# Performance work log

Hardware: AMD Instinct MI355X
Metric: run time of the kernel (lower is better)

The kernel has to match this reference:

```python
import jax, jax.numpy as jnp
import numpy as np

GROUPS = 4
RATIO = 2


def setup_inputs() -> dict:
    key = jax.random.key(0)
    k1, k2, k3 = jax.random.split(key, 3)
    B, C, H, W = 16, 256, 64, 64
    c_out = 2 * GROUPS * RATIO ** 2  # 32
    x = jax.random.normal(k1, (B, C, H, W), dtype=jnp.float32)
    # offset conv: normal_init std=0.001 (full 1x1 conv)
    w_off = jax.random.normal(k2, (c_out, C), dtype=jnp.float32) * 0.001
    b_off = jnp.zeros((c_out,), dtype=jnp.float32)
    # scope conv: grouped 1x1 (groups=4); init is zeros in the module, use tiny
    # random values so sigmoid != exactly 0.5 and the path is exercised
    w_scope = jax.random.normal(k3, (GROUPS, c_out // GROUPS, C // GROUPS), dtype=jnp.float32) * 0.001
    b_scope = jnp.zeros((c_out,), dtype=jnp.float32)
    return {"x": x, "w_off": w_off, "b_off": b_off, "w_scope": w_scope, "b_scope": b_scope}


def _pixel_shuffle(t, r):
    B, C, H, W = t.shape
    Co = C // (r * r)
    t = t.reshape(B, Co, r, r, H, W)
    t = t.transpose(0, 1, 4, 2, 5, 3)  # B, Co, H, r, W, r
    return t.reshape(B, Co, H * r, W * r)


def _bilinear_border(img, ix, iy):
    # img: (c, H, W); ix, iy: (Ho, Wo) pixel coords in input space
    c, H, W = img.shape
    ix = jnp.clip(ix, 0.0, W - 1.0)  # border padding: clamp coordinate
    iy = jnp.clip(iy, 0.0, H - 1.0)
    x0f = jnp.floor(ix)
    y0f = jnp.floor(iy)
    wx = ix - x0f
    wy = iy - y0f
    x0 = jnp.clip(x0f.astype(jnp.int32), 0, W - 1)
    x1 = jnp.clip(x0 + 1, 0, W - 1)
    y0 = jnp.clip(y0f.astype(jnp.int32), 0, H - 1)
    y1 = jnp.clip(y0 + 1, 0, H - 1)
    v00 = img[:, y0, x0]
    v01 = img[:, y0, x1]
    v10 = img[:, y1, x0]
    v11 = img[:, y1, x1]
    return (v00 * (1 - wy) * (1 - wx) + v01 * (1 - wy) * wx
            + v10 * wy * (1 - wx) + v11 * wy * wx)


def reference(x, w_off, b_off, w_scope, b_scope):
    B, C, H, W = x.shape
    g, r = GROUPS, RATIO
    # offset 1x1 conv
    off = jnp.einsum('bihw,oi->bohw', x, w_off) + b_off[None, :, None, None]
    # grouped scope 1x1 conv + sigmoid scaling
    xgc = x.reshape(B, g, C // g, H, W)
    sc = jnp.einsum('bgihw,goi->bgohw', xgc, w_scope).reshape(B, -1, H, W)
    sc = sc + b_scope[None, :, None, None]
    off = jax.nn.sigmoid(sc) * 0.5 * off
    # pixel shuffle to (B, 2*g, Ho, Wo)
    off = _pixel_shuffle(off, r)
    Ho, Wo = H * r, W * r
    # rearrange: x 'b (c grp) h w -> (b grp) c h w'; offset 'b (grp two) h w -> (b grp) h w two'
    cg = C // g
    xg = x.reshape(B, cg, g, H, W).transpose(0, 2, 1, 3, 4).reshape(B * g, cg, H, W)
    og = off.reshape(B, g, 2, Ho, Wo).transpose(0, 1, 3, 4, 2).reshape(B * g, Ho, Wo, 2)
    # sampling grid: centers + offset, normalized by (Wo, Ho), align_corners=False
    posx = jnp.linspace(0.5, Wo - 0.5, Wo, dtype=x.dtype)[None, :]   # (1, Wo)
    posy = jnp.linspace(0.5, Ho - 0.5, Ho, dtype=x.dtype)[:, None]   # (Ho, 1)
    gx = 2.0 * (posx + og[..., 0]) / Wo - 1.0  # (B*g, Ho, Wo)
    gy = 2.0 * (posy + og[..., 1]) / Ho - 1.0
    # unnormalize (align_corners=False): pix = ((g+1)*size - 1) / 2
    ix = ((gx + 1.0) * W - 1.0) * 0.5
    iy = ((gy + 1.0) * H - 1.0) * 0.5
    out = jax.vmap(_bilinear_border)(xg, ix, iy)  # (B*g, cg, Ho, Wo)
    # rearrange back: '(b grp) c h w -> b (c grp) h w'
    out = out.reshape(B, g, cg, Ho, Wo).transpose(0, 2, 1, 3, 4).reshape(B, C, Ho, Wo)
    return out
```

## Files before the change

### kernel.cpp

```cpp
#include <hip/hip_runtime.h>
#include <math.h>

#define B_   16
#define C_   256
#define H_   64
#define W_   64
#define G_   4
#define HO_  128
#define WO_  128
#define HW_  (H_ * W_)
#define HOWO_ (HO_ * WO_)

__constant__ float wconst[8 * 32 * 40];

__global__ __launch_bounds__(256) void prep_kernel(
    const float* __restrict__ w_off,
    const float* __restrict__ w_scope,
    float* __restrict__ wout)
{
    const int k = blockIdx.x * 256 + threadIdx.x;
    if (k >= 8 * 32 * 40) return;
    const int q  = k % 40;
    const int r  = k / 40;
    const int i2 = r & 31;
    const int u  = r >> 5;
    const int v  = u & 3;
    const int hi = u >> 2;
    const int i  = 64 * v + 32 * hi + i2;
    float val;
    if (q < 32) val = w_off[q * 256 + i];
    else        val = w_scope[v * 512 + (q - 32) * 64 + 32 * hi + i2];
    wout[k] = val;
}

__global__ __launch_bounds__(512, 6) void fused_kernel(
    const float* __restrict__ x,
    const float* __restrict__ b_off,
    const float* __restrict__ b_scope,
    float* __restrict__ out)
{
    __shared__ float4 red[8][8][64];
    __shared__ float4 aux[8][64];

    const int tid = threadIdx.x;
    const int u   = __builtin_amdgcn_readfirstlane(tid >> 6);
    const int w   = tid & 63;

    const int bid = ((blockIdx.x & 7) << 7) | (blockIdx.x >> 3);
    const int h   = bid & 63;
    const int b   = bid >> 6;

    const int v   = u & 3;
    const int hi  = u >> 2;

    const float* xq = x + (size_t)b * C_ * HW_ +
                      (size_t)(64 * v + 32 * hi) * HW_ + h * W_ + w;
    const int wbase0 = u * (32 * 40);

    float offp[32];
    float scp[8];
#pragma unroll
    for (int j = 0; j < 32; ++j) offp[j] = 0.f;
#pragma unroll
    for (int j = 0; j < 8; ++j) scp[j] = 0.f;

#pragma unroll 4
    for (int i2 = 0; i2 < 32; ++i2) {
        const float xv = xq[(size_t)i2 * HW_];
        const int wb = wbase0 + i2 * 40;
#pragma unroll
        for (int j = 0; j < 32; ++j) offp[j] += xv * wconst[wb + j];
#pragma unroll
        for (int j = 0; j < 8; ++j)  scp[j] += xv * wconst[wb + 32 + j];
    }

    if (hi) {
#pragma unroll
        for (int j = 0; j < 8; ++j)
            red[4 + v][j][w] = make_float4(offp[4 * j + 0], offp[4 * j + 1],
                                           offp[4 * j + 2], offp[4 * j + 3]);
        aux[2 * v + 0][w] = make_float4(scp[0], scp[1], scp[2], scp[3]);
        aux[2 * v + 1][w] = make_float4(scp[4], scp[5], scp[6], scp[7]);
    }
    __syncthreads();
    if (!hi) {
#pragma unroll
        for (int j = 0; j < 8; ++j) {
            const float4 p = red[4 + v][j][w];
            offp[4 * j + 0] += p.x; offp[4 * j + 1] += p.y;
            offp[4 * j + 2] += p.z; offp[4 * j + 3] += p.w;
        }
        const float4 s0 = aux[2 * v + 0][w];
        const float4 s1 = aux[2 * v + 1][w];
        scp[0] += s0.x; scp[1] += s0.y; scp[2] += s0.z; scp[3] += s0.w;
        scp[4] += s1.x; scp[5] += s1.y; scp[6] += s1.z; scp[7] += s1.w;
#pragma unroll
        for (int j = 0; j < 8; ++j)
            red[v][j][w] = make_float4(offp[4 * j + 0], offp[4 * j + 1],
                                       offp[4 * j + 2], offp[4 * j + 3]);
    }
    __syncthreads();
    if (!hi) {
        float4 a = make_float4(0.f, 0.f, 0.f, 0.f);
        float4 c = make_float4(0.f, 0.f, 0.f, 0.f);
#pragma unroll
        for (int tt = 0; tt < 4; ++tt) {
            const float4 pa = red[tt][2 * v + 0][w];
            const float4 pc = red[tt][2 * v + 1][w];
            a.x += pa.x; a.y += pa.y; a.z += pa.z; a.w += pa.w;
            c.x += pc.x; c.y += pc.y; c.z += pc.z; c.w += pc.w;
        }
        const float ao[8] = {a.x, a.y, a.z, a.w, c.x, c.y, c.z, c.w};
        float f[8];
#pragma unroll
        for (int j = 0; j < 8; ++j) {
            const float offv = ao[j] + b_off[8 * v + j];
            const float scv  = scp[j] + b_scope[8 * v + j];
            f[j] = offv * 0.5f / (1.f + expf(-scv));
        }
#pragma unroll
        for (int r1 = 0; r1 < 2; ++r1) {
            const float hoF = (float)(2 * h + r1);
            float ix0 = ((float)(2 * w + 0) - 0.5f + f[2 * r1 + 0]) * 0.5f;
            float iy0 = (hoF - 0.5f + f[4 + 2 * r1 + 0]) * 0.5f;
            float ix1 = ((float)(2 * w + 1) - 0.5f + f[2 * r1 + 1]) * 0.5f;
            float iy1 = (hoF - 0.5f + f[4 + 2 * r1 + 1]) * 0.5f;
            ix0 = fminf(fmaxf(ix0, 0.f), (float)(W_ - 1));
            iy0 = fminf(fmaxf(iy0, 0.f), (float)(H_ - 1));
            ix1 = fminf(fmaxf(ix1, 0.f), (float)(W_ - 1));
            iy1 = fminf(fmaxf(iy1, 0.f), (float)(H_ - 1));
            aux[2 * v + r1][w] = make_float4(ix0, iy0, ix1, iy1);
        }
    }
    __syncthreads();

    const int wo = tid & 127;
    const int z  = (tid >> 7) & 1;
    const int gh = tid >> 8;
    const int ho = 2 * h + z;

    const float2* cbase = (const float2*)&aux[0][0];
    const float* xb0 = x + (size_t)b * C_ * HW_;
    float* ob0 = out + (size_t)b * C_ * HOWO_ + ho * WO_ + wo;

#pragma unroll
    for (int gg = 0; gg < 2; ++gg) {
        const int g = 2 * gh + gg;
        const float2 c = cbase[(g * 2 + z) * 128 + wo];
        const float ix = c.x, iy = c.y;

        const float x0f = floorf(ix);
        const float y0f = floorf(iy);
        const float wx = ix - x0f;
        const float wy = iy - y0f;
        int x0 = (int)x0f;
        int y0 = (int)y0f;
        x0 = max(0, min(x0, W_ - 1));
        y0 = max(0, min(y0, H_ - 1));
        const int x1 = min(x0 + 1, W_ - 1);
        const int y1 = min(y0 + 1, H_ - 1);

        const float w00 = (1.f - wy) * (1.f - wx);
        const float w01 = (1.f - wy) * wx;
        const float w10 = wy * (1.f - wx);
        const float w11 = wy * wx;

        const int p00 = y0 * W_ + x0;
        const int p01 = y0 * W_ + x1;
        const int p10 = y1 * W_ + x0;
        const int p11 = y1 * W_ + x1;

        const float* xb = xb0 + (size_t)g * HW_;
        float* ob = ob0 + (size_t)g * HOWO_;

#pragma unroll 4
        for (int cc = 0; cc < 64; ++cc) {
            const float* pl = xb + (size_t)cc * 4 * HW_;
            const float val = pl[p00] * w00 + pl[p01] * w01 +
                              pl[p10] * w10 + pl[p11] * w11;
            __builtin_nontemporal_store(val, &ob[(size_t)cc * 4 * HOWO_]);
        }
    }
}

extern "C" void kernel_launch(void* const* d_in, const int* in_sizes, int n_in,
                              void* d_out, int out_size, void* d_ws, size_t ws_size,
                              hipStream_t stream) {
    const float* x       = (const float*)d_in[0];
    const float* w_off   = (const float*)d_in[1];
    const float* b_off   = (const float*)d_in[2];
    const float* w_scope = (const float*)d_in[3];
    const float* b_scope = (const float*)d_in[4];
    float* out = (float*)d_out;

    void* wsym = nullptr;
    (void)hipGetSymbolAddress(&wsym, HIP_SYMBOL(wconst));

    prep_kernel<<<dim3(40), 256, 0, stream>>>(w_off, w_scope, (float*)wsym);
    fused_kernel<<<dim3(B_ * H_), 512, 0, stream>>>(x, b_off, b_scope, out);
}
```

Measured before the change: 78.41 us.

## Split fused kernel into conv-coordinate kernel and separate sampling kernel

The single fused kernel is split in two. The first computes the offset and scope convolutions and writes the clamped sampling coordinates to a workspace buffer. The second kernel runs more, smaller blocks (one per batch, group and output row pair) to do the bilinear gather and write the output. This decouples the compute-bound conv phase from the memory-bound gather phase so each can have its own occupancy and grid shape, at the cost of an extra launch and a workspace round trip for the coordinates.

```diff
diff --git a/kernel.cpp b/kernel.cpp
--- a/kernel.cpp
+++ b/kernel.cpp
@@ -33,11 +33,11 @@
     wout[k] = val;
 }
 
-__global__ __launch_bounds__(512, 6) void fused_kernel(
+__global__ __launch_bounds__(512, 6) void conv_kernel(
     const float* __restrict__ x,
     const float* __restrict__ b_off,
     const float* __restrict__ b_scope,
-    float* __restrict__ out)
+    float2* __restrict__ coords)
 {
     __shared__ float4 red[8][8][64];
     __shared__ float4 aux[8][64];
@@ -129,57 +129,62 @@
             iy0 = fminf(fmaxf(iy0, 0.f), (float)(H_ - 1));
             ix1 = fminf(fmaxf(ix1, 0.f), (float)(W_ - 1));
             iy1 = fminf(fmaxf(iy1, 0.f), (float)(H_ - 1));
-            aux[2 * v + r1][w] = make_float4(ix0, iy0, ix1, iy1);
-        }
-    }
-    __syncthreads();
-
-    const int wo = tid & 127;
-    const int z  = (tid >> 7) & 1;
-    const int gh = tid >> 8;
-    const int ho = 2 * h + z;
-
-    const float2* cbase = (const float2*)&aux[0][0];
-    const float* xb0 = x + (size_t)b * C_ * HW_;
-    float* ob0 = out + (size_t)b * C_ * HOWO_ + ho * WO_ + wo;
-
-#pragma unroll
-    for (int gg = 0; gg < 2; ++gg) {
-        const int g = 2 * gh + gg;
-        const float2 c = cbase[(g * 2 + z) * 128 + wo];
-        const float ix = c.x, iy = c.y;
-
-        const float x0f = floorf(ix);
-        const float y0f = floorf(iy);
-        const float wx = ix - x0f;
-        const float wy = iy - y0f;
-        int x0 = (int)x0f;
-        int y0 = (int)y0f;
-        x0 = max(0, min(x0, W_ - 1));
-        y0 = max(0, min(y0, H_ - 1));
-        const int x1 = min(x0 + 1, W_ - 1);
-        const int y1 = min(y0 + 1, H_ - 1);
-
-        const float w00 = (1.f - wy) * (1.f - wx);
-        const float w01 = (1.f - wy) * wx;
-        const float w10 = wy * (1.f - wx);
-        const float w11 = wy * wx;
-
-        const int p00 = y0 * W_ + x0;
-        const int p01 = y0 * W_ + x1;
-        const int p10 = y1 * W_ + x0;
-        const int p11 = y1 * W_ + x1;
-
-        const float* xb = xb0 + (size_t)g * HW_;
-        float* ob = ob0 + (size_t)g * HOWO_;
+            float4* cw = (float4*)&coords[(((size_t)b * G_ + v) * HO_ +
+                                           (2 * h + r1)) * WO_ + 2 * w];
+            *cw = make_float4(ix0, iy0, ix1, iy1);
+        }
+    }
+}
+
+__global__ __launch_bounds__(256) void sample_kernel(
+    const float* __restrict__ x,
+    const float2* __restrict__ coords,
+    float* __restrict__ out)
+{
+    const int xcd = blockIdx.x & 7;
+    const int r   = blockIdx.x >> 3;
+    const int b   = 2 * xcd + (r >> 8);
+    const int g   = (r >> 6) & 3;
+    const int hp  = r & 63;
+
+    const int wo = threadIdx.x & 127;
+    const int z  = threadIdx.x >> 7;
+    const int ho = 2 * hp + z;
+
+    const float2 c = coords[(((size_t)b * G_ + g) * HO_ + ho) * WO_ + wo];
+    const float ix = c.x, iy = c.y;
+
+    const float x0f = floorf(ix);
+    const float y0f = floorf(iy);
+    const float wx = ix - x0f;
+    const float wy = iy - y0f;
+    int x0 = (int)x0f;
+    int y0 = (int)y0f;
+    x0 = max(0, min(x0, W_ - 1));
+    y0 = max(0, min(y0, H_ - 1));
+    const int x1 = min(x0 + 1, W_ - 1);
+    const int y1 = min(y0 + 1, H_ - 1);
+
+    const float w00 = (1.f - wy) * (1.f - wx);
+    const float w01 = (1.f - wy) * wx;
+    const float w10 = wy * (1.f - wx);
+    const float w11 = wy * wx;
+
+    const int p00 = y0 * W_ + x0;
+    const int p01 = y0 * W_ + x1;
+    const int p10 = y1 * W_ + x0;
+    const int p11 = y1 * W_ + x1;
+
+    const float* xb = x + (size_t)b * C_ * HW_ + (size_t)g * HW_;
+    float* ob = out + (size_t)b * C_ * HOWO_ + (size_t)g * HOWO_ +
+                ho * WO_ + wo;
 
 #pragma unroll 4
-        for (int cc = 0; cc < 64; ++cc) {
-            const float* pl = xb + (size_t)cc * 4 * HW_;
-            const float val = pl[p00] * w00 + pl[p01] * w01 +
-                              pl[p10] * w10 + pl[p11] * w11;
-            __builtin_nontemporal_store(val, &ob[(size_t)cc * 4 * HOWO_]);
-        }
+    for (int cc = 0; cc < 64; ++cc) {
+        const float* pl = xb + (size_t)cc * 4 * HW_;
+        const float v = pl[p00] * w00 + pl[p01] * w01 +
+                        pl[p10] * w10 + pl[p11] * w11;
+        __builtin_nontemporal_store(v, &ob[(size_t)cc * 4 * HOWO_]);
     }
 }
 
@@ -192,10 +197,12 @@
     const float* w_scope = (const float*)d_in[3];
     const float* b_scope = (const float*)d_in[4];
     float* out = (float*)d_out;
+    float2* coords = (float2*)d_ws;
 
     void* wsym = nullptr;
     (void)hipGetSymbolAddress(&wsym, HIP_SYMBOL(wconst));
 
     prep_kernel<<<dim3(40), 256, 0, stream>>>(w_off, w_scope, (float*)wsym);
-    fused_kernel<<<dim3(B_ * H_), 512, 0, stream>>>(x, b_off, b_scope, out);
-}
+    conv_kernel<<<dim3(B_ * H_), 512, 0, stream>>>(x, b_off, b_scope, coords);
+    sample_kernel<<<dim3(4096), 256, 0, stream>>>(x, coords, out);
+}
```

Measured after the change: 99.22 us. 26.5% more time.
